# Kernel tuning notes

Measured on AMD Instinct MI355X. Metric: run time of the kernel, lower is better.

Reference implementation:

```python
import jax, jax.numpy as jnp
import numpy as np

N_NODES = 50000


def gcn_conv(x, src, dst, norm, W, b, n_nodes):
    """One GCNConv layer: out = scatter_add(norm * (x @ W)[src] -> dst) + b.
    src/dst already include self loops; norm is the symmetric D^-1/2 A_hat D^-1/2 edge weight."""
    h = x @ W  # [N, C_out]
    msg = h[src] * norm[:, None]  # [E+N, C_out]
    out = jax.ops.segment_sum(msg, dst, num_segments=n_nodes)
    return out + b


def build_norm(edge_index, n_nodes):
    """Add self loops and compute symmetric GCN normalization (PyG GCNConv default)."""
    loop = jnp.arange(n_nodes, dtype=edge_index.dtype)
    src = jnp.concatenate([edge_index[0], loop])
    dst = jnp.concatenate([edge_index[1], loop])
    deg = jax.ops.segment_sum(jnp.ones_like(dst, dtype=jnp.float32), dst, num_segments=n_nodes)
    dinv = jnp.where(deg > 0, jax.lax.rsqrt(jnp.maximum(deg, 1.0)), 0.0)
    norm = dinv[src] * dinv[dst]
    return src, dst, norm


def setup_inputs() -> dict:
    key = jax.random.key(0)
    ks = jax.random.split(key, 8)
    in_c, h1, h2, out_c = 768, 256, 128, 2
    x = jax.random.normal(ks[0], (N_NODES, in_c), dtype=jnp.float32)
    edge_index = jax.random.randint(ks[1], (2, 800000), 0, N_NODES, dtype=jnp.int32)
    W1 = jax.random.normal(ks[2], (in_c, h1), dtype=jnp.float32) * 0.02
    b1 = jnp.zeros((h1,), dtype=jnp.float32)
    W2 = jax.random.normal(ks[3], (h1, h2), dtype=jnp.float32) * 0.02
    b2 = jnp.zeros((h2,), dtype=jnp.float32)
    W3 = jax.random.normal(ks[4], (h2, out_c), dtype=jnp.float32) * 0.02
    b3 = jnp.zeros((out_c,), dtype=jnp.float32)
    return {"x": x, "edge_index": edge_index, "W1": W1, "b1": b1,
            "W2": W2, "b2": b2, "W3": W3, "b3": b3}


def reference(x, edge_index, W1, b1, W2, b2, W3, b3):
    n = x.shape[0]
    src, dst, norm = build_norm(edge_index, n)
    # Dropout is identity in eval mode (training=False), so it is omitted.
    h = jax.nn.relu(gcn_conv(x, src, dst, norm, W1, b1, n))
    h = jax.nn.relu(gcn_conv(h, src, dst, norm, W2, b2, n))
    h = gcn_conv(h, src, dst, norm, W3, b3, n)
    return jax.nn.sigmoid(h)
```

## Files before the change

kernel.cpp:

```cpp
#include <hip/hip_runtime.h>
#include <math.h>

typedef short s16x8 __attribute__((ext_vector_type(8)));
typedef __bf16 b16x8 __attribute__((ext_vector_type(8)));
typedef float f32x4 __attribute__((ext_vector_type(4)));
typedef float f32x2 __attribute__((ext_vector_type(2)));
typedef unsigned int u32x4 __attribute__((ext_vector_type(4)));

__device__ inline short f2bf(float f) {
    unsigned u = __float_as_uint(f);
    unsigned r = u + 0x7FFFu + ((u >> 16) & 1u);
    return (short)(r >> 16);
}
__device__ inline float bf2f(unsigned short u) {
    return __uint_as_float(((unsigned)u) << 16);
}


__device__ inline void make_wt_elem(const float* __restrict__ W, short* __restrict__ Wt,
                                    int K, int N, int idx) {
    int NB = N >> 7;
    int j = idx & 7;
    int l = (idx >> 3) & 63;
    int nt = (idx >> 9) & 7;
    int rest = idx >> 12;
    int b = rest % NB;
    int c = rest / NB;
    int k = c * 32 + (l >> 4) * 8 + j;
    int n = b * 128 + nt * 16 + (l & 15);
    Wt[idx] = f2bf(W[(size_t)k * N + n]);
}

__global__ void prep_kernel(const int* __restrict__ dst, int* __restrict__ cnt, int E,
                            const float* __restrict__ W1, short* __restrict__ Wt1,
                            const float* __restrict__ W2, short* __restrict__ Wt2,
                            int cb, int w1b) {
    int b = blockIdx.x;
    int tid = threadIdx.x;
    if (b < cb) {
        int e = b * 256 + tid;
        if (e < E) atomicAdd(&cnt[dst[e]], 1);
    } else if (b < cb + w1b) {
        int idx = (b - cb) * 256 + tid;
        make_wt_elem(W1, Wt1, 768, 256, idx);
    } else {
        int idx = (b - cb - w1b) * 256 + tid;
        make_wt_elem(W2, Wt2, 256, 128, idx);
    }
}


__global__ __launch_bounds__(1024) void blockscan_kernel(const int* __restrict__ cnt,
                                                         int* __restrict__ rp,
                                                         int* __restrict__ bsum, int n) {
    __shared__ int sdata[1024];
    int tid = threadIdx.x;
    int i = blockIdx.x * 1024 + tid;
    int v = (i < n) ? cnt[i] : 0;
    sdata[tid] = v;
    __syncthreads();
    for (int off = 1; off < 1024; off <<= 1) {
        int t = 0;
        if (tid >= off) t = sdata[tid - off];
        __syncthreads();
        sdata[tid] += t;
        __syncthreads();
    }
    if (i < n) rp[i] = sdata[tid] - v;
    if (tid == 1023) bsum[blockIdx.x] = sdata[1023];
}

__global__ void topscan_kernel(int* bsum, int nb) {
    int lane = threadIdx.x;
    int carry = 0;
    for (int base = 0; base < nb; base += 64) {
        int idx = base + lane;
        int orig = (idx < nb) ? bsum[idx] : 0;
        int v = orig;
        for (int off = 1; off < 64; off <<= 1) {
            int t = __shfl_up(v, off, 64);
            if (lane >= off) v += t;
        }
        if (idx < nb) bsum[idx] = carry + v - orig;
        carry += __shfl(v, 63, 64);
    }
}

__global__ __launch_bounds__(1024) void fixup_kernel(int* __restrict__ rp,
                                                     const int* __restrict__ bsum,
                                                     const int* __restrict__ cnt,
                                                     int* __restrict__ cursor,
                                                     float* __restrict__ dinv,
                                                     int n, int E) {
    int i = blockIdx.x * 1024 + threadIdx.x;
    if (i < n) {
        int r = rp[i] + bsum[blockIdx.x];
        rp[i] = r;
        cursor[i] = r;
        dinv[i] = rsqrtf((float)cnt[i] + 1.0f);
    }
    if (i == 0) rp[n] = E;
}

__global__ void fill_kernel(const int* __restrict__ src, const int* __restrict__ dst,
                            int* __restrict__ cursor, const float* __restrict__ dinv,
                            int* __restrict__ csrc, float* __restrict__ cw, int E) {
    int e = blockIdx.x * blockDim.x + threadIdx.x;
    if (e >= E) return;
    int d = dst[e];
    int s = src[e];
    int p = atomicAdd(&cursor[d], 1);
    csrc[p] = s;
    cw[p] = dinv[s] * dinv[d];
}


__global__ __launch_bounds__(256, 3) void gemm1_kernel(const float* __restrict__ x,
                                                       const short* __restrict__ Wt,
                                                       unsigned char* __restrict__ h8,
                                                       int M) {
    constexpr int KC = 24;
    constexpr int RT = 2;
    constexpr int O = KC * 4;
    constexpr int F = KC * RT * 64 / 256;

    __shared__ s16x8 As[KC * RT * 64];

    const int tid = threadIdx.x;
    const int m0 = blockIdx.x * (RT * 16);

    s16x8 v[F];
#pragma unroll
    for (int i = 0; i < F; ++i) {
        int idx = i * 256 + tid;
        int r = idx / O;
        int o = idx - r * O;
        int row = m0 + r;
        if (row >= M) row = M - 1;
        const float4* fp = (const float4*)(x + (size_t)row * 768 + o * 8);
        float4 f0 = fp[0];
        float4 f1 = fp[1];
        u32x4 pk;
        pk.x = (__float_as_uint(f0.x) >> 16) | (__float_as_uint(f0.y) & 0xFFFF0000u);
        pk.y = (__float_as_uint(f0.z) >> 16) | (__float_as_uint(f0.w) & 0xFFFF0000u);
        pk.z = (__float_as_uint(f1.x) >> 16) | (__float_as_uint(f1.y) & 0xFFFF0000u);
        pk.w = (__float_as_uint(f1.z) >> 16) | (__float_as_uint(f1.w) & 0xFFFF0000u);
        v[i] = __builtin_bit_cast(s16x8, pk);
    }
#pragma unroll
    for (int i = 0; i < F; ++i) {
        int idx = i * 256 + tid;
        int r = idx / O;
        int o = idx - r * O;
        int c = o >> 2, q = o & 3;
        int slot = q * 16 + (((r & 15) + q + ((c & 3) << 2)) & 15);
        As[(c * RT + (r >> 4)) * 64 + slot] = v[i];
    }
    __syncthreads();

    const int lane = tid & 63;
    const int wave = tid >> 6;
    const int b128 = wave >> 1;
    const int nt0 = (wave & 1) * 4;
    const int q = lane >> 4;
    const int rl = lane & 15;
    const s16x8* wt = (const s16x8*)Wt;

    f32x4 acc[RT][4];
#pragma unroll
    for (int i = 0; i < RT; ++i)
#pragma unroll
        for (int j = 0; j < 4; ++j)
            acc[i][j] = (f32x4){0.f, 0.f, 0.f, 0.f};

#pragma unroll 4
    for (int c = 0; c < KC; ++c) {
        int slot = q * 16 + ((rl + q + ((c & 3) << 2)) & 15);
        b16x8 areg[RT], breg[4];
#pragma unroll
        for (int i = 0; i < RT; ++i)
            areg[i] = __builtin_bit_cast(b16x8, As[(c * RT + i) * 64 + slot]);
        size_t bb = (size_t)(c * 2 + b128) * 512 + nt0 * 64 + lane;
#pragma unroll
        for (int j = 0; j < 4; ++j)
            breg[j] = __builtin_bit_cast(b16x8, wt[bb + j * 64]);
#pragma unroll
        for (int i = 0; i < RT; ++i)
#pragma unroll
            for (int j = 0; j < 4; ++j)
                acc[i][j] = __builtin_amdgcn_mfma_f32_16x16x32_bf16(areg[i], breg[j], acc[i][j], 0, 0, 0);
    }

    const int quad = lane >> 4;
    const int nl = lane & 15;
#pragma unroll
    for (int i = 0; i < RT; ++i) {
        int rbase = m0 + i * 16 + quad * 4;
#pragma unroll
        for (int j = 0; j < 4; ++j) {
            int col = wave * 64 + j * 16 + nl;
#pragma unroll
            for (int r = 0; r < 4; ++r) {
                int row = rbase + r;
                if (row < M) {
                    unsigned u = __builtin_amdgcn_cvt_pk_fp8_f32(acc[i][j][r], acc[i][j][r], 0, false);
                    h8[(size_t)row * 256 + col] = (unsigned char)(u & 0xFF);
                }
            }
        }
    }
}


template<typename AT, int KC, int RT, int CW, int MINW>
__global__ __launch_bounds__(256, MINW) void gemm_panel_kernel(
        const AT* __restrict__ A, const short* __restrict__ Wt,
        unsigned short* __restrict__ Cb, int M) {
    constexpr int K = KC * 32;
    constexpr int O = KC * 4;
    constexpr int F = KC * RT / 4;
    constexpr int NCOLS = CW * 64;
    constexpr int NB = NCOLS >> 7;
    constexpr int MT = RT * CW / 4;

    __shared__ s16x8 As[KC * RT * 64];

    const int tid = threadIdx.x;
    const int m0 = blockIdx.x * (RT * 16);

    s16x8 v[F];
#pragma unroll
    for (int i = 0; i < F; ++i) {
        int idx = i * 256 + tid;
        int r = idx / O;
        int o = idx - r * O;
        int row = m0 + r;
        if (row >= M) row = M - 1;
        v[i] = *(const s16x8*)((const unsigned short*)A + (size_t)row * K + o * 8);
    }
#pragma unroll
    for (int i = 0; i < F; ++i) {
        int idx = i * 256 + tid;
        int r = idx / O;
        int o = idx - r * O;
        int c = o >> 2, q = o & 3;
        int slot = q * 16 + (((r & 15) + q + ((c & 3) << 2)) & 15);
        As[(c * RT + (r >> 4)) * 64 + slot] = v[i];
    }
    __syncthreads();

    const int lane = tid & 63;
    const int wave = tid >> 6;
    const int cw_i = wave % CW;
    const int rg = wave / CW;
    const int mtb = rg * MT;
    const int b128 = (cw_i * 64) >> 7;
    const int nt0 = (cw_i * 4) & 7;
    const int q = lane >> 4;
    const int rl = lane & 15;
    const s16x8* wt = (const s16x8*)Wt;

    f32x4 acc[MT][4];
#pragma unroll
    for (int i = 0; i < MT; ++i)
#pragma unroll
        for (int j = 0; j < 4; ++j)
            acc[i][j] = (f32x4){0.f, 0.f, 0.f, 0.f};

#pragma unroll 4
    for (int c = 0; c < KC; ++c) {
        int slot = q * 16 + ((rl + q + ((c & 3) << 2)) & 15);
        b16x8 areg[MT], breg[4];
#pragma unroll
        for (int i = 0; i < MT; ++i)
            areg[i] = __builtin_bit_cast(b16x8, As[(c * RT + mtb + i) * 64 + slot]);
        size_t bb = (size_t)(c * NB + b128) * 512 + nt0 * 64 + lane;
#pragma unroll
        for (int j = 0; j < 4; ++j)
            breg[j] = __builtin_bit_cast(b16x8, wt[bb + j * 64]);
#pragma unroll
        for (int i = 0; i < MT; ++i)
#pragma unroll
            for (int j = 0; j < 4; ++j)
                acc[i][j] = __builtin_amdgcn_mfma_f32_16x16x32_bf16(areg[i], breg[j], acc[i][j], 0, 0, 0);
    }

    const int quad = lane >> 4;
    const int nl = lane & 15;
#pragma unroll
    for (int i = 0; i < MT; ++i) {
        int rbase = m0 + (mtb + i) * 16 + quad * 4;
#pragma unroll
        for (int j = 0; j < 4; ++j) {
            int col = cw_i * 64 + j * 16 + nl;
#pragma unroll
            for (int rr = 0; rr < 4; ++rr) {
                int row = rbase + rr;
                if (row < M) Cb[(size_t)row * NCOLS + col] = (unsigned short)f2bf(acc[i][j][rr]);
            }
        }
    }
}


__global__ __launch_bounds__(256) void agg256_f8_kernel(const unsigned char* __restrict__ h8,
                                                        const int* __restrict__ rp,
                                                        const int* __restrict__ csrc,
                                                        const float* __restrict__ cw,
                                                        const float* __restrict__ dinv,
                                                        const float* __restrict__ bias,
                                                        unsigned short* __restrict__ out, int n) {
    int node = blockIdx.x * 4 + (threadIdx.x >> 6);
    int lane = threadIdx.x & 63;
    if (node >= n) return;
    const unsigned* hp = (const unsigned*)h8;
    float di = dinv[node];
    float ws = di * di;
    unsigned sv = hp[(size_t)node * 64 + lane];
    f32x2 slo = __builtin_amdgcn_cvt_pk_f32_fp8(sv, false);
    f32x2 shi = __builtin_amdgcn_cvt_pk_f32_fp8(sv, true);
    float a0 = ws * slo.x, a1 = ws * slo.y, a2 = ws * shi.x, a3 = ws * shi.y;
    int e = rp[node], e1 = rp[node + 1];
    for (; e + 1 < e1; e += 2) {
        int s0 = csrc[e], s1 = csrc[e + 1];
        float w0 = cw[e], w1 = cw[e + 1];
        unsigned v0 = hp[(size_t)s0 * 64 + lane];
        unsigned v1 = hp[(size_t)s1 * 64 + lane];
        f32x2 l0 = __builtin_amdgcn_cvt_pk_f32_fp8(v0, false);
        f32x2 h0 = __builtin_amdgcn_cvt_pk_f32_fp8(v0, true);
        f32x2 l1 = __builtin_amdgcn_cvt_pk_f32_fp8(v1, false);
        f32x2 h1 = __builtin_amdgcn_cvt_pk_f32_fp8(v1, true);
        a0 += w0 * l0.x + w1 * l1.x;
        a1 += w0 * l0.y + w1 * l1.y;
        a2 += w0 * h0.x + w1 * h1.x;
        a3 += w0 * h0.y + w1 * h1.y;
    }
    if (e < e1) {
        int s0 = csrc[e];
        float w0 = cw[e];
        unsigned v0 = hp[(size_t)s0 * 64 + lane];
        f32x2 l0 = __builtin_amdgcn_cvt_pk_f32_fp8(v0, false);
        f32x2 h0 = __builtin_amdgcn_cvt_pk_f32_fp8(v0, true);
        a0 += w0 * l0.x; a1 += w0 * l0.y; a2 += w0 * h0.x; a3 += w0 * h0.y;
    }
    float4 bv = *(const float4*)&bias[lane * 4];
    a0 = fmaxf(a0 + bv.x, 0.f); a1 = fmaxf(a1 + bv.y, 0.f);
    a2 = fmaxf(a2 + bv.z, 0.f); a3 = fmaxf(a3 + bv.w, 0.f);
    ushort4 ov;
    ov.x = (unsigned short)f2bf(a0); ov.y = (unsigned short)f2bf(a1);
    ov.z = (unsigned short)f2bf(a2); ov.w = (unsigned short)f2bf(a3);
    ((ushort4*)out)[(size_t)node * 64 + lane] = ov;
}

__global__ __launch_bounds__(256) void agg128_w3_kernel(const unsigned short* __restrict__ h,
                                                        const int* __restrict__ rp,
                                                        const int* __restrict__ csrc,
                                                        const float* __restrict__ cw,
                                                        const float* __restrict__ dinv,
                                                        const float* __restrict__ b2,
                                                        const float* __restrict__ W3,
                                                        float* __restrict__ z, int n) {
    int node = blockIdx.x * 4 + (threadIdx.x >> 6);
    int lane = threadIdx.x & 63;
    if (node >= n) return;
    const unsigned* hp = (const unsigned*)h;
    float di = dinv[node];
    float ws = di * di;
    unsigned sv = hp[(size_t)node * 64 + lane];
    float a0 = ws * __uint_as_float(sv << 16);
    float a1 = ws * __uint_as_float(sv & 0xFFFF0000u);
    int e = rp[node], e1 = rp[node + 1];
    for (; e + 1 < e1; e += 2) {
        int s0 = csrc[e], s1 = csrc[e + 1];
        float w0 = cw[e], w1 = cw[e + 1];
        unsigned v0 = hp[(size_t)s0 * 64 + lane];
        unsigned v1 = hp[(size_t)s1 * 64 + lane];
        a0 += w0 * __uint_as_float(v0 << 16) + w1 * __uint_as_float(v1 << 16);
        a1 += w0 * __uint_as_float(v0 & 0xFFFF0000u) + w1 * __uint_as_float(v1 & 0xFFFF0000u);
    }
    if (e < e1) {
        int s0 = csrc[e];
        float w0 = cw[e];
        unsigned v0 = hp[(size_t)s0 * 64 + lane];
        a0 += w0 * __uint_as_float(v0 << 16);
        a1 += w0 * __uint_as_float(v0 & 0xFFFF0000u);
    }
    float2 bv = *(const float2*)&b2[lane * 2];
    a0 = fmaxf(a0 + bv.x, 0.f);
    a1 = fmaxf(a1 + bv.y, 0.f);
    float4 wv = *(const float4*)&W3[lane * 4];
    float z0 = a0 * wv.x + a1 * wv.z;
    float z1 = a0 * wv.y + a1 * wv.w;
    for (int off = 32; off > 0; off >>= 1) {
        z0 += __shfl_down(z0, off, 64);
        z1 += __shfl_down(z1, off, 64);
    }
    if (lane == 0) {
        z[2 * (size_t)node] = z0;
        z[2 * (size_t)node + 1] = z1;
    }
}

__global__ void agg3_kernel(const float* __restrict__ z, const int* __restrict__ rp,
                            const int* __restrict__ csrc, const float* __restrict__ cw,
                            const float* __restrict__ dinv, const float* __restrict__ bias,
                            float* __restrict__ out, int n) {
    int node = blockIdx.x * blockDim.x + threadIdx.x;
    if (node >= n) return;
    float di = dinv[node];
    float a0 = di * di * z[2 * (size_t)node];
    float a1 = di * di * z[2 * (size_t)node + 1];
    int e1 = rp[node + 1];
    for (int e = rp[node]; e < e1; ++e) {
        int s = csrc[e];
        float w = cw[e];
        a0 += w * z[2 * (size_t)s];
        a1 += w * z[2 * (size_t)s + 1];
    }
    a0 += bias[0];
    a1 += bias[1];
    out[2 * (size_t)node]     = 1.f / (1.f + __expf(-a0));
    out[2 * (size_t)node + 1] = 1.f / (1.f + __expf(-a1));
}


extern "C" void kernel_launch(void* const* d_in, const int* in_sizes, int n_in,
                              void* d_out, int out_size, void* d_ws, size_t ws_size,
                              hipStream_t stream) {
    const float* x  = (const float*)d_in[0];
    const int*   ei = (const int*)d_in[1];
    const float* W1 = (const float*)d_in[2];
    const float* b1 = (const float*)d_in[3];
    const float* W2 = (const float*)d_in[4];
    const float* b2 = (const float*)d_in[5];
    const float* W3 = (const float*)d_in[6];
    const float* b3 = (const float*)d_in[7];
    float* out = (float*)d_out;

    const int E  = in_sizes[1] / 2;
    const int C1 = in_sizes[3];
    const int C2 = in_sizes[5];
    const int K1 = in_sizes[2] / C1;
    const int N  = in_sizes[0] / K1;

    const int* srcv = ei;
    const int* dstv = ei + E;

    char* p = (char*)d_ws;
    auto carve = [&](size_t bytes) {
        char* r = p;
        p += (bytes + 255) & ~(size_t)255;
        return r;
    };
    int*   cnt    = (int*)carve((size_t)N * 4);
    int*   rp     = (int*)carve((size_t)(N + 1) * 4);
    int*   cursor = (int*)carve((size_t)N * 4);
    float* dinv   = (float*)carve((size_t)N * 4);
    int*   bsum   = (int*)carve(1024 * 4);
    int*   csrc   = (int*)carve((size_t)E * 4);
    float* cw     = (float*)carve((size_t)E * 4);
    short* Wt1    = (short*)carve((size_t)K1 * C1 * 2);
    short* Wt2    = (short*)carve((size_t)C1 * C2 * 2);
    unsigned char* h8 = (unsigned char*)carve((size_t)N * C1);
    unsigned short* hB = (unsigned short*)carve((size_t)N * C1 * 2);
    unsigned short* h2 = (unsigned short*)carve((size_t)N * C2 * 2);
    float* zbuf   = (float*)carve((size_t)N * 2 * 4);

    const int nb = (N + 1023) / 1024;
    const int cb = (E + 255) / 256;
    const int w1b = (K1 * C1) / 256;
    const int w2b = (C1 * C2) / 256;

    hipMemsetAsync(cnt, 0, (size_t)N * 4, stream);
    prep_kernel<<<cb + w1b + w2b, 256, 0, stream>>>(dstv, cnt, E, W1, Wt1, W2, Wt2, cb, w1b);
    blockscan_kernel<<<nb, 1024, 0, stream>>>(cnt, rp, bsum, N);
    topscan_kernel<<<1, 64, 0, stream>>>(bsum, nb);
    fixup_kernel<<<nb, 1024, 0, stream>>>(rp, bsum, cnt, cursor, dinv, N, E);
    fill_kernel<<<(E + 255) / 256, 256, 0, stream>>>(srcv, dstv, cursor, dinv, csrc, cw, E);

    gemm1_kernel<<<(N + 31) / 32, 256, 0, stream>>>(x, Wt1, h8, N);
    agg256_f8_kernel<<<(N + 3) / 4, 256, 0, stream>>>(h8, rp, csrc, cw, dinv, b1, hB, N);

    gemm_panel_kernel<unsigned short, 8, 4, 2, 4><<<(N + 63) / 64, 256, 0, stream>>>(hB, Wt2, h2, N);
    agg128_w3_kernel<<<(N + 3) / 4, 256, 0, stream>>>(h2, rp, csrc, cw, dinv, b2, W3, zbuf, N);

    agg3_kernel<<<(N + 255) / 256, 256, 0, stream>>>(zbuf, rp, csrc, cw, dinv, b3, out, N);
}
```

Before: 488.4 us.

## Split each wavefront into four edge groups with 16-byte gathers in aggregation kernels

Both row-aggregation kernels now split the 64-lane wavefront into four groups of 16 lanes. Each group processes a different edge at the same time and loads 16 bytes per lane instead of 4. Edge indices and weights are loaded cooperatively, 64 at a time, and broadcast with shuffles, so the per-edge scalar loads are gone. The aim is more memory-level parallelism and wider loads for the gather. The cost is a cross-group shuffle reduction at the end, more registers for the accumulators, and idle lanes on the output store.

```diff
diff --git a/kernel.cpp b/kernel.cpp
--- a/kernel.cpp
+++ b/kernel.cpp
@@ -313,43 +313,67 @@
     int node = blockIdx.x * 4 + (threadIdx.x >> 6);
     int lane = threadIdx.x & 63;
     if (node >= n) return;
-    const unsigned* hp = (const unsigned*)h8;
+    const int eg = lane >> 4;
+    const int ch = lane & 15;
     float di = dinv[node];
-    float ws = di * di;
-    unsigned sv = hp[(size_t)node * 64 + lane];
-    f32x2 slo = __builtin_amdgcn_cvt_pk_f32_fp8(sv, false);
-    f32x2 shi = __builtin_amdgcn_cvt_pk_f32_fp8(sv, true);
-    float a0 = ws * slo.x, a1 = ws * slo.y, a2 = ws * shi.x, a3 = ws * shi.y;
-    int e = rp[node], e1 = rp[node + 1];
-    for (; e + 1 < e1; e += 2) {
-        int s0 = csrc[e], s1 = csrc[e + 1];
-        float w0 = cw[e], w1 = cw[e + 1];
-        unsigned v0 = hp[(size_t)s0 * 64 + lane];
-        unsigned v1 = hp[(size_t)s1 * 64 + lane];
-        f32x2 l0 = __builtin_amdgcn_cvt_pk_f32_fp8(v0, false);
-        f32x2 h0 = __builtin_amdgcn_cvt_pk_f32_fp8(v0, true);
-        f32x2 l1 = __builtin_amdgcn_cvt_pk_f32_fp8(v1, false);
-        f32x2 h1 = __builtin_amdgcn_cvt_pk_f32_fp8(v1, true);
-        a0 += w0 * l0.x + w1 * l1.x;
-        a1 += w0 * l0.y + w1 * l1.y;
-        a2 += w0 * h0.x + w1 * h1.x;
-        a3 += w0 * h0.y + w1 * h1.y;
-    }
-    if (e < e1) {
-        int s0 = csrc[e];
-        float w0 = cw[e];
-        unsigned v0 = hp[(size_t)s0 * 64 + lane];
-        f32x2 l0 = __builtin_amdgcn_cvt_pk_f32_fp8(v0, false);
-        f32x2 h0 = __builtin_amdgcn_cvt_pk_f32_fp8(v0, true);
-        a0 += w0 * l0.x; a1 += w0 * l0.y; a2 += w0 * h0.x; a3 += w0 * h0.y;
-    }
-    float4 bv = *(const float4*)&bias[lane * 4];
-    a0 = fmaxf(a0 + bv.x, 0.f); a1 = fmaxf(a1 + bv.y, 0.f);
-    a2 = fmaxf(a2 + bv.z, 0.f); a3 = fmaxf(a3 + bv.w, 0.f);
-    ushort4 ov;
-    ov.x = (unsigned short)f2bf(a0); ov.y = (unsigned short)f2bf(a1);
-    ov.z = (unsigned short)f2bf(a2); ov.w = (unsigned short)f2bf(a3);
-    ((ushort4*)out)[(size_t)node * 64 + lane] = ov;
+
+    float acc[16];
+    {
+        u32x4 v = *(const u32x4*)(h8 + (size_t)node * 256 + ch * 16);
+        float ws = (eg == 0) ? di * di : 0.f;
+#pragma unroll
+        for (int u = 0; u < 4; ++u) {
+            f32x2 lo = __builtin_amdgcn_cvt_pk_f32_fp8(v[u], false);
+            f32x2 hi = __builtin_amdgcn_cvt_pk_f32_fp8(v[u], true);
+            acc[u * 4 + 0] = ws * lo.x; acc[u * 4 + 1] = ws * lo.y;
+            acc[u * 4 + 2] = ws * hi.x; acc[u * 4 + 3] = ws * hi.y;
+        }
+    }
+
+    int e0 = rp[node], e1 = rp[node + 1];
+    for (int base = e0; base < e1; base += 64) {
+        int idx = base + lane;
+        int sb = (idx < e1) ? csrc[idx] : 0;
+        float wb = (idx < e1) ? cw[idx] : 0.f;
+        int cnt = e1 - base; if (cnt > 64) cnt = 64;
+#pragma unroll 2
+        for (int i = 0; i < cnt; i += 4) {
+            int s = __shfl(sb, i + eg, 64);
+            float w = __shfl(wb, i + eg, 64);
+            u32x4 v = *(const u32x4*)(h8 + (size_t)s * 256 + ch * 16);
+#pragma unroll
+            for (int u = 0; u < 4; ++u) {
+                f32x2 lo = __builtin_amdgcn_cvt_pk_f32_fp8(v[u], false);
+                f32x2 hi = __builtin_amdgcn_cvt_pk_f32_fp8(v[u], true);
+                acc[u * 4 + 0] += w * lo.x; acc[u * 4 + 1] += w * lo.y;
+                acc[u * 4 + 2] += w * hi.x; acc[u * 4 + 3] += w * hi.y;
+            }
+        }
+    }
+
+#pragma unroll
+    for (int k = 0; k < 16; ++k) {
+        acc[k] += __shfl_xor(acc[k], 16, 64);
+        acc[k] += __shfl_xor(acc[k], 32, 64);
+    }
+
+    unsigned pk[8];
+#pragma unroll
+    for (int k = 0; k < 8; ++k) {
+        float4 bv;
+        float b0 = bias[ch * 16 + 2 * k];
+        float b1 = bias[ch * 16 + 2 * k + 1];
+        float a0 = fmaxf(acc[2 * k] + b0, 0.f);
+        float a1 = fmaxf(acc[2 * k + 1] + b1, 0.f);
+        pk[k] = ((unsigned)(unsigned short)f2bf(a0)) | (((unsigned)(unsigned short)f2bf(a1)) << 16);
+        (void)bv;
+    }
+    if (eg < 2) {
+        u32x4 ov;
+        ov.x = pk[eg * 4 + 0]; ov.y = pk[eg * 4 + 1];
+        ov.z = pk[eg * 4 + 2]; ov.w = pk[eg * 4 + 3];
+        *(u32x4*)((char*)out + (size_t)node * 512 + ch * 32 + eg * 16) = ov;
+    }
 }
 
 __global__ __launch_bounds__(256) void agg128_w3_kernel(const unsigned short* __restrict__ h,
@@ -363,37 +387,56 @@
     int node = blockIdx.x * 4 + (threadIdx.x >> 6);
     int lane = threadIdx.x & 63;
     if (node >= n) return;
-    const unsigned* hp = (const unsigned*)h;
+    const int eg = lane >> 4;
+    const int ch = lane & 15;
     float di = dinv[node];
-    float ws = di * di;
-    unsigned sv = hp[(size_t)node * 64 + lane];
-    float a0 = ws * __uint_as_float(sv << 16);
-    float a1 = ws * __uint_as_float(sv & 0xFFFF0000u);
-    int e = rp[node], e1 = rp[node + 1];
-    for (; e + 1 < e1; e += 2) {
-        int s0 = csrc[e], s1 = csrc[e + 1];
-        float w0 = cw[e], w1 = cw[e + 1];
-        unsigned v0 = hp[(size_t)s0 * 64 + lane];
-        unsigned v1 = hp[(size_t)s1 * 64 + lane];
-        a0 += w0 * __uint_as_float(v0 << 16) + w1 * __uint_as_float(v1 << 16);
-        a1 += w0 * __uint_as_float(v0 & 0xFFFF0000u) + w1 * __uint_as_float(v1 & 0xFFFF0000u);
-    }
-    if (e < e1) {
-        int s0 = csrc[e];
-        float w0 = cw[e];
-        unsigned v0 = hp[(size_t)s0 * 64 + lane];
-        a0 += w0 * __uint_as_float(v0 << 16);
-        a1 += w0 * __uint_as_float(v0 & 0xFFFF0000u);
-    }
-    float2 bv = *(const float2*)&b2[lane * 2];
-    a0 = fmaxf(a0 + bv.x, 0.f);
-    a1 = fmaxf(a1 + bv.y, 0.f);
-    float4 wv = *(const float4*)&W3[lane * 4];
-    float z0 = a0 * wv.x + a1 * wv.z;
-    float z1 = a0 * wv.y + a1 * wv.w;
-    for (int off = 32; off > 0; off >>= 1) {
-        z0 += __shfl_down(z0, off, 64);
-        z1 += __shfl_down(z1, off, 64);
+
+    float acc[8];
+    {
+        u32x4 v = *(const u32x4*)((const char*)h + (size_t)node * 256 + ch * 16);
+        float ws = (eg == 0) ? di * di : 0.f;
+#pragma unroll
+        for (int u = 0; u < 4; ++u) {
+            acc[u * 2 + 0] = ws * __uint_as_float(v[u] << 16);
+            acc[u * 2 + 1] = ws * __uint_as_float(v[u] & 0xFFFF0000u);
+        }
+    }
+
+    int e0 = rp[node], e1 = rp[node + 1];
+    for (int base = e0; base < e1; base += 64) {
+        int idx = base + lane;
+        int sb = (idx < e1) ? csrc[idx] : 0;
+        float wb = (idx < e1) ? cw[idx] : 0.f;
+        int cnt = e1 - base; if (cnt > 64) cnt = 64;
+#pragma unroll 2
+        for (int i = 0; i < cnt; i += 4) {
+            int s = __shfl(sb, i + eg, 64);
+            float w = __shfl(wb, i + eg, 64);
+            u32x4 v = *(const u32x4*)((const char*)h + (size_t)s * 256 + ch * 16);
+#pragma unroll
+            for (int u = 0; u < 4; ++u) {
+                acc[u * 2 + 0] += w * __uint_as_float(v[u] << 16);
+                acc[u * 2 + 1] += w * __uint_as_float(v[u] & 0xFFFF0000u);
+            }
+        }
+    }
+
+#pragma unroll
+    for (int k = 0; k < 8; ++k) {
+        acc[k] += __shfl_xor(acc[k], 16, 64);
+        acc[k] += __shfl_xor(acc[k], 32, 64);
+    }
+
+    float z0 = 0.f, z1 = 0.f;
+#pragma unroll
+    for (int k = 0; k < 8; ++k) {
+        float a = fmaxf(acc[k] + b2[ch * 8 + k], 0.f);
+        z0 += a * W3[(ch * 8 + k) * 2];
+        z1 += a * W3[(ch * 8 + k) * 2 + 1];
+    }
+    for (int off = 8; off > 0; off >>= 1) {
+        z0 += __shfl_xor(z0, off, 64);
+        z1 += __shfl_xor(z1, off, 64);
     }
     if (lane == 0) {
         z[2 * (size_t)node] = z0;
```

Result: faster. 443.0 us (-9.3%).
